# Kernel tuning notes

Hardware: AMD Instinct MI355X
Metric: run time of the kernel (lower is better)

Reference implementation:

```python
import jax, jax.numpy as jnp
import numpy as np

DIM_PN = 64
N_P = 16
BN_EPS = 1e-5


def _conv1x1(h, w, b):
    # h: (B, Cin, N), w: (Cout, Cin), b: (Cout,)
    return jnp.einsum('oc,bcn->bon', w, h) + b[None, :, None]


def _bn(h, g, be):
    # training-mode BatchNorm1d: stats over (batch, points)
    m = h.mean(axis=(0, 2), keepdims=True)
    v = h.var(axis=(0, 2), keepdims=True)
    return (h - m) * jax.lax.rsqrt(v + BN_EPS) * g[None, :, None] + be[None, :, None]


def setup_inputs() -> dict:
    key = jax.random.key(0)
    ks = jax.random.split(key, 8)
    B, N = 32, 16384
    x = jax.random.normal(ks[0], (B, 3, N), dtype=jnp.float32)
    def kaiming(k, shape):
        fan_in = shape[1]
        return jax.random.normal(k, shape, dtype=jnp.float32) * np.float32(1.0 / np.sqrt(fan_in))
    w1 = kaiming(ks[1], (64, 3));   b1 = jnp.zeros((64,), jnp.float32)
    w2 = kaiming(ks[2], (128, 64)); b2 = jnp.zeros((128,), jnp.float32)
    w3 = kaiming(ks[3], (DIM_PN, 128)); b3 = jnp.zeros((DIM_PN,), jnp.float32)
    g1 = jnp.ones((64,), jnp.float32); be1 = jnp.zeros((64,), jnp.float32)
    g2 = jnp.ones((128,), jnp.float32); be2 = jnp.zeros((128,), jnp.float32)
    g3 = jnp.ones((DIM_PN,), jnp.float32); be3 = jnp.zeros((DIM_PN,), jnp.float32)
    return {"x": x, "w1": w1, "b1": b1, "g1": g1, "be1": be1,
            "w2": w2, "b2": b2, "g2": g2, "be2": be2,
            "w3": w3, "b3": b3, "g3": g3, "be3": be3}


def reference(x, w1, b1, g1, be1, w2, b2, g2, be2, w3, b3, g3, be3):
    # SoftPoolfeat forward (core of MSN), vectorized SoftPool.
    h = jax.nn.relu(_bn(_conv1x1(x, w1, b1), g1, be1))       # (B,64,N)
    h = jax.nn.relu(_bn(_conv1x1(h, w2, b2), g2, be2))       # (B,128,N)
    h = _bn(_conv1x1(h, w3, b3), g3, be3)                    # (B,C=64,N)
    # SoftPool: per channel c, ascending sort order over points, keep first N_p.
    idx = jnp.argsort(h, axis=2)[:, :, :N_P]                 # (B,C,Np) int32
    # sp_cube[b, c2, c, n] = h[b, c2, idx[b, c, n]]
    sp_cube = jnp.take_along_axis(h[:, :, None, :], idx[:, None, :, :], axis=3)  # (B,C,C,Np)
    # partial[b, ch, c, n] = x[b, ch, idx[b, c, n]]  (original repeats x over featdim then gathers)
    partial = jnp.take_along_axis(x[:, :, None, :], idx[:, None, :, :], axis=3)  # (B,3,C,Np)
    feat = jnp.concatenate([partial, sp_cube], axis=1)       # (B,3+C,C,Np)
    sp_idx = jnp.broadcast_to(idx[:, None, :, :], (idx.shape[0], 3, idx.shape[1], idx.shape[2]))
    return feat, sp_idx
```

## Files before the change

kernel.cpp:

```cpp
#include <hip/hip_runtime.h>
#include <cstddef>

#pragma clang fp contract(off)

#define B_    32
#define N_    16384
#define NPTS  (B_ * N_)
#define FEATSZ (32 * 67 * 64 * 16)
#define NCHUNK (NPTS / 64)
#define GRID_Y2 1024
#define GRID_XS 512

enum : int {
  D_X9    = 0,
  D_Y3SUM = 16,
  D_Y3SQ  = 80,
  D_Y2S   = 144,
  D_Y2Q   = 272,
  D_XPART = 1024,
};
enum : int {
  F_M1   = 16384,
  F_R1   = 16448,
  F_M2   = 16512,
  F_R2   = 16640,
  F_M3   = 16768,
  F_R3   = 16832,
  F_W2T  = 16896,
  F_W3T  = 25088,
  F_TOPK = 33280,
};
#define Y3_B     524288
#define Y2PART_B 524288

__device__ __forceinline__ float h1_of(const float* __restrict__ w1,
                                       const float* __restrict__ b1,
                                       const float* __restrict__ g1,
                                       const float* __restrict__ be1,
                                       const float* __restrict__ fw, int c,
                                       float x0, float x1, float x2) {
  float s = w1[c*3+0] * x0;
  s = fmaf(w1[c*3+1], x1, s);
  s = fmaf(w1[c*3+2], x2, s);
  float y1 = s + b1[c];
  float t = y1 - fw[F_M1 + c];
  float u = t * fw[F_R1 + c];
  u = u * g1[c];
  u = u + be1[c];
  return fmaxf(u, 0.f);
}

__global__ __launch_bounds__(256) void k_xstats64(const float* __restrict__ x,
                                                  double* __restrict__ wd) {
  __shared__ double sacc[4][9];
  double a0=0,a1=0,a2=0,m00=0,m01=0,m02=0,m11=0,m12=0,m22=0;
  for (int p = blockIdx.x * 256 + threadIdx.x; p < NPTS; p += gridDim.x * 256) {
    int b = p >> 14, n = p & (N_ - 1);
    const float* xb = x + (size_t)b * 3 * N_ + n;
    double x0 = xb[0], x1 = xb[N_], x2 = xb[2 * N_];
    a0 += x0; a1 += x1; a2 += x2;
    m00 = fma(x0,x0,m00); m01 = fma(x0,x1,m01); m02 = fma(x0,x2,m02);
    m11 = fma(x1,x1,m11); m12 = fma(x1,x2,m12); m22 = fma(x2,x2,m22);
  }
  #pragma unroll
  for (int m = 32; m >= 1; m >>= 1) {
    a0 += __shfl_xor(a0, m); a1 += __shfl_xor(a1, m); a2 += __shfl_xor(a2, m);
    m00 += __shfl_xor(m00, m); m01 += __shfl_xor(m01, m); m02 += __shfl_xor(m02, m);
    m11 += __shfl_xor(m11, m); m12 += __shfl_xor(m12, m); m22 += __shfl_xor(m22, m);
  }
  const int wv = threadIdx.x >> 6;
  if ((threadIdx.x & 63) == 0) {
    sacc[wv][0] = a0;  sacc[wv][1] = a1;  sacc[wv][2] = a2;
    sacc[wv][3] = m00; sacc[wv][4] = m01; sacc[wv][5] = m02;
    sacc[wv][6] = m11; sacc[wv][7] = m12; sacc[wv][8] = m22;
  }
  __syncthreads();
  if (threadIdx.x < 9) {
    double s = ((sacc[0][threadIdx.x] + sacc[1][threadIdx.x])
              + sacc[2][threadIdx.x]) + sacc[3][threadIdx.x];
    wd[D_XPART + blockIdx.x * 9 + threadIdx.x] = s;
  }
}

__global__ __launch_bounds__(64) void k_redX(double* __restrict__ wd) {
  int j = threadIdx.x;
  if (j >= 9) return;
  double s = 0.0;
  for (int b = 0; b < GRID_XS; ++b) s += wd[D_XPART + b * 9 + j];
  wd[D_X9 + j] = s;
}

__global__ void k_prep1(const float* __restrict__ w1, const float* __restrict__ b1,
                        double* __restrict__ wd, float* __restrict__ fw) {
  int c = threadIdx.x;
  if (c >= 64) return;
  const double inv = 1.0 / (double)NPTS;
  double mx0 = wd[0]*inv, mx1 = wd[1]*inv, mx2 = wd[2]*inv;
  double c00 = wd[3]*inv - mx0*mx0, c01 = wd[4]*inv - mx0*mx1, c02 = wd[5]*inv - mx0*mx2;
  double c11 = wd[6]*inv - mx1*mx1, c12 = wd[7]*inv - mx1*mx2, c22 = wd[8]*inv - mx2*mx2;
  double w0 = w1[c*3+0], w1_ = w1[c*3+1], w2_ = w1[c*3+2];
  double m1 = w0*mx0 + w1_*mx1 + w2_*mx2 + (double)b1[c];
  double var = w0*w0*c00 + w1_*w1_*c11 + w2_*w2_*c22
             + 2.0*(w0*w1_*c01 + w0*w2_*c02 + w1_*w2_*c12);
  fw[F_M1 + c] = (float)m1;
  float vpe = (float)var + 1e-5f;
  fw[F_R1 + c] = (float)(1.0 / sqrt((double)vpe));
}

__global__ __launch_bounds__(64) void k_prepW(const float* __restrict__ w2,
                                              const float* __restrict__ w3,
                                              float* __restrict__ fw) {
  const int o = blockIdx.x, c = threadIdx.x;
  fw[F_W2T + c * 128 + o] = w2[o * 64 + c];
  fw[F_W3T + o * 64 + c] = w3[c * 128 + o];
}

__global__ __launch_bounds__(1024, 8) void k_y2stats(const float* __restrict__ x,
                                                     const float* __restrict__ w1,
                                                     const float* __restrict__ b1,
                                                     const float* __restrict__ g1,
                                                     const float* __restrict__ be1,
                                                     const float* __restrict__ fw,
                                                     double* __restrict__ y2part) {
  __shared__ float h1g[16][64][4];
  const int tid = threadIdx.x;
  const int lane = tid & 63;
  const int wvu = __builtin_amdgcn_readfirstlane(tid >> 6);
  const int o0 = wvu * 8;
  const float* w2t = fw + F_W2T;
  double s64[8], q64[8];
  #pragma unroll
  for (int j = 0; j < 8; ++j) { s64[j] = 0.0; q64[j] = 0.0; }

  for (int chunk = blockIdx.x; chunk < NCHUNK; chunk += GRID_Y2) {
    __syncthreads();
    {
      int p = chunk * 64 + lane;
      int b = p >> 14, n = p & (N_ - 1);
      const float* xb = x + (size_t)b * 3 * N_ + n;
      float x0 = xb[0], x1 = xb[N_], x2 = xb[2 * N_];
      const int c0 = wvu * 4;
      float hv[4];
      #pragma unroll
      for (int k = 0; k < 4; ++k) hv[k] = h1_of(w1, b1, g1, be1, fw, c0 + k, x0, x1, x2);
      float4 v; v.x = hv[0]; v.y = hv[1]; v.z = hv[2]; v.w = hv[3];
      *(float4*)&h1g[wvu][lane][0] = v;
    }
    __syncthreads();
    float acc[8];
    #pragma unroll
    for (int j = 0; j < 8; ++j) acc[j] = 0.f;
    #pragma unroll 4
    for (int cg = 0; cg < 16; ++cg) {
      float4 hgv = *(const float4*)&h1g[cg][lane][0];
      float hx[4] = {hgv.x, hgv.y, hgv.z, hgv.w};
      #pragma unroll
      for (int e = 0; e < 4; ++e) {
        const int c = cg * 4 + e;
        const float hc = hx[e];
        const float* wc = w2t + c * 128 + o0;
        #pragma unroll
        for (int j = 0; j < 8; ++j) acc[j] = fmaf(wc[j], hc, acc[j]);
      }
    }
    #pragma unroll
    for (int j = 0; j < 8; ++j) {
      double v = (double)acc[j];
      s64[j] += v;
      q64[j] = fma(v, v, q64[j]);
    }
  }
  #pragma unroll
  for (int j = 0; j < 8; ++j) {
    #pragma unroll
    for (int m = 32; m >= 1; m >>= 1) {
      s64[j] += __shfl_xor(s64[j], m);
      q64[j] += __shfl_xor(q64[j], m);
    }
  }
  if (lane == 0) {
    #pragma unroll
    for (int j = 0; j < 8; ++j) {
      int o = o0 + j;
      y2part[((size_t)blockIdx.x * 128 + o) * 2 + 0] = s64[j];
      y2part[((size_t)blockIdx.x * 128 + o) * 2 + 1] = q64[j];
    }
  }
}

__global__ __launch_bounds__(256) void k_redY2(const double* __restrict__ y2part,
                                               double* __restrict__ wd) {
  __shared__ double ss[256], sq[256];
  const int o = blockIdx.x, tid = threadIdx.x;
  double s = 0.0, q = 0.0;
  for (int blk = tid; blk < GRID_Y2; blk += 256) {
    s += y2part[((size_t)blk * 128 + o) * 2 + 0];
    q += y2part[((size_t)blk * 128 + o) * 2 + 1];
  }
  ss[tid] = s; sq[tid] = q;
  __syncthreads();
  for (int st = 128; st > 0; st >>= 1) {
    if (tid < st) { ss[tid] += ss[tid + st]; sq[tid] += sq[tid + st]; }
    __syncthreads();
  }
  if (tid == 0) { wd[D_Y2S + o] = ss[0]; wd[D_Y2Q + o] = sq[0]; }
}

__global__ void k_prep2s(const float* __restrict__ b2,
                         double* __restrict__ wd, float* __restrict__ fw) {
  int o = threadIdx.x;
  if (o >= 128) return;
  const double inv = 1.0 / (double)NPTS;
  double mraw = wd[D_Y2S + o] * inv;
  double var = wd[D_Y2Q + o] * inv - mraw * mraw;
  fw[F_M2 + o] = (float)(mraw + (double)b2[o]);
  float vpe = (float)var + 1e-5f;
  fw[F_R2 + o] = (float)(1.0 / sqrt((double)vpe));
}

__global__ __launch_bounds__(512, 4) void k_fwd(const float* __restrict__ x,
                                                const float* __restrict__ w1,
                                                const float* __restrict__ b1,
                                                const float* __restrict__ g1,
                                                const float* __restrict__ be1,
                                                const float* __restrict__ b2,
                                                const float* __restrict__ g2,
                                                const float* __restrict__ be2,
                                                const float* __restrict__ b3,
                                                const float* __restrict__ fw,
                                                float* __restrict__ y3out,
                                                int pbase) {
  __shared__ float h1g[16][64][4];
  __shared__ float h2g[16][64][4];
  const int tid = threadIdx.x;
  const int lane = tid & 63;
  const int wvu = __builtin_amdgcn_readfirstlane(tid >> 6);
  const int p = pbase + blockIdx.x * 64 + lane;
  const int b = p >> 14, n = p & (N_ - 1);
  const float* xb = x + (size_t)b * 3 * N_ + n;
  const float x0 = xb[0], x1 = xb[N_], x2 = xb[2 * N_];
  const float* w2t = fw + F_W2T;
  const float* w3t = fw + F_W3T;
  const int q0 = wvu * 8;
  float a3[8];

  {
    const int c0 = wvu * 8;
    float hv[8];
    #pragma unroll
    for (int k = 0; k < 8; ++k) hv[k] = h1_of(w1, b1, g1, be1, fw, c0 + k, x0, x1, x2);
    #pragma unroll
    for (int gq = 0; gq < 2; ++gq) {
      float4 v; v.x = hv[gq*4+0]; v.y = hv[gq*4+1]; v.z = hv[gq*4+2]; v.w = hv[gq*4+3];
      *(float4*)&h1g[(c0 >> 2) + gq][lane][0] = v;
    }
  }
  __syncthreads();

  #pragma unroll
  for (int H = 0; H < 2; ++H) {
    {
      const int o0 = H * 64 + wvu * 8;
      float acc[8];
      #pragma unroll
      for (int j = 0; j < 8; ++j) acc[j] = 0.f;
      #pragma unroll 4
      for (int cg = 0; cg < 16; ++cg) {
        float4 hgv = *(const float4*)&h1g[cg][lane][0];
        float hx[4] = {hgv.x, hgv.y, hgv.z, hgv.w};
        #pragma unroll
        for (int e = 0; e < 4; ++e) {
          const int c = cg * 4 + e;
          const float hc = hx[e];
          const float* wc = w2t + c * 128 + o0;
          #pragma unroll
          for (int j = 0; j < 8; ++j) acc[j] = fmaf(wc[j], hc, acc[j]);
        }
      }
      float hv2[8];
      #pragma unroll
      for (int j = 0; j < 8; ++j) {
        int o = o0 + j;
        float y2 = acc[j] + b2[o];
        float t = y2 - fw[F_M2 + o];
        float u = t * fw[F_R2 + o];
        u = u * g2[o];
        u = u + be2[o];
        hv2[j] = fmaxf(u, 0.f);
      }
      #pragma unroll
      for (int gq = 0; gq < 2; ++gq) {
        float4 v; v.x = hv2[gq*4+0]; v.y = hv2[gq*4+1]; v.z = hv2[gq*4+2]; v.w = hv2[gq*4+3];
        *(float4*)&h2g[wvu * 2 + gq][lane][0] = v;
      }
    }
    __syncthreads();
    {
      #pragma unroll 4
      for (int og = 0; og < 16; ++og) {
        float4 hgv = *(const float4*)&h2g[og][lane][0];
        float hx[4] = {hgv.x, hgv.y, hgv.z, hgv.w};
        #pragma unroll
        for (int e = 0; e < 4; ++e) {
          const int o = H * 64 + og * 4 + e;
          const float ho = hx[e];
          const float* wr = w3t + o * 64 + q0;
          if (H == 0 && og == 0 && e == 0) {
            #pragma unroll
            for (int j = 0; j < 8; ++j) a3[j] = wr[j] * ho;
          } else {
            #pragma unroll
            for (int j = 0; j < 8; ++j) a3[j] = fmaf(wr[j], ho, a3[j]);
          }
        }
      }
    }
    __syncthreads();
  }

  float* yrow = y3out + (size_t)b * 64 * N_ + n;
  #pragma unroll
  for (int j = 0; j < 8; ++j) {
    int q = q0 + j;
    yrow[(size_t)q * N_] = a3[j] + b3[q];
  }
}

__global__ void k_prep3(double* __restrict__ wd, float* __restrict__ fw) {
  int o = threadIdx.x;
  if (o >= 64) return;
  const double inv = 1.0 / (double)NPTS;
  double m = wd[D_Y3SUM + o] * inv;
  double var = wd[D_Y3SQ + o] * inv - m * m;
  fw[F_M3 + o] = (float)m;
  float vpe = (float)var + 1e-5f;
  fw[F_R3 + o] = (float)(1.0 / sqrt((double)vpe));
}

__global__ __launch_bounds__(256) void k_topk(const float* __restrict__ y3,
                                              const float* __restrict__ g3,
                                              int* __restrict__ topk,
                                              double* __restrict__ wd) {
  __shared__ float sval[256 * 16];
  __shared__ int   sidx[256 * 16];
  __shared__ double ssum[256], ssq[256];
  const int tid = threadIdx.x;
  const int row = blockIdx.x;
  const int c = row & 63;
  const float sgn = (g3[c] >= 0.f) ? 1.f : -1.f;
  const float4* y = (const float4*)(y3 + (size_t)row * N_);
  float val[16]; int idx[16];
  #pragma unroll
  for (int k = 0; k < 16; ++k) { val[k] = 3.0e38f; idx[k] = 0x7fffffff; }
  auto ins = [&](float v, int i) {
    if (v < val[15] || (v == val[15] && i < idx[15])) {
      float cv = v; int ci = i;
      #pragma unroll
      for (int k = 0; k < 16; ++k) {
        bool sw = (cv < val[k]) || (cv == val[k] && ci < idx[k]);
        float tv = val[k]; int tj = idx[k];
        if (sw) { val[k] = cv; idx[k] = ci; cv = tv; ci = tj; }
      }
    }
  };
  double s = 0.0, q = 0.0;
  #pragma unroll 1
  for (int it = 0; it < 16; ++it) {
    int n4 = it * 256 + tid;
    float4 v = y[n4];
    int nb = n4 * 4;
    {
      double a = v.x, bb = v.y, cc2 = v.z, d = v.w;
      s += a + bb + cc2 + d;
      q = fma(a,a,q); q = fma(bb,bb,q); q = fma(cc2,cc2,q); q = fma(d,d,q);
    }
    ins(sgn * v.x, nb + 0);
    ins(sgn * v.y, nb + 1);
    ins(sgn * v.z, nb + 2);
    ins(sgn * v.w, nb + 3);
  }
  ssum[tid] = s; ssq[tid] = q;
  #pragma unroll
  for (int k = 0; k < 16; ++k) { sval[tid*16+k] = val[k]; sidx[tid*16+k] = idx[k]; }
  __syncthreads();
  for (int st = 128; st > 0; st >>= 1) {
    if (tid < st) { ssum[tid] += ssum[tid + st]; ssq[tid] += ssq[tid + st]; }
    __syncthreads();
  }
  if (tid == 0) {
    atomicAdd(&wd[D_Y3SUM + c], ssum[0]);
    atomicAdd(&wd[D_Y3SQ  + c], ssq[0]);
  }
  for (int st2 = 1; st2 < 256; st2 <<= 1) {
    if ((tid & (2 * st2 - 1)) == 0) {
      int pa = tid * 16, pb = (tid + st2) * 16;
      int ia = 0, ib = 0;
      float mv[16]; int mi[16];
      #pragma unroll
      for (int k = 0; k < 16; ++k) {
        float va = sval[pa + ia]; int ja = sidx[pa + ia];
        float vb = sval[pb + ib]; int jb = sidx[pb + ib];
        bool ta = (va < vb) || (va == vb && ja < jb);
        mv[k] = ta ? va : vb; mi[k] = ta ? ja : jb;
        if (ta) ++ia; else ++ib;
      }
      #pragma unroll
      for (int k = 0; k < 16; ++k) { sval[pa + k] = mv[k]; sidx[pa + k] = mi[k]; }
    }
    __syncthreads();
  }
  if (tid < 16) topk[row * 16 + tid] = sidx[tid];
}

__global__ __launch_bounds__(256) void k_gather(const float* __restrict__ x,
                                                const float* __restrict__ fw,
                                                const float* __restrict__ g3,
                                                const float* __restrict__ be3,
                                                const float* __restrict__ y3,
                                                const int* __restrict__ topk,
                                                float* __restrict__ out) {
  __shared__ int s_i[16];
  __shared__ float s_m[64], s_r[64], s_g[64], s_b[64];
  const int tid = threadIdx.x;
  const int row = blockIdx.x;
  const int b = row >> 6, c = row & 63;
  if (tid < 16) s_i[tid] = topk[row * 16 + tid];
  if (tid < 64) {
    s_m[tid] = fw[F_M3 + tid]; s_r[tid] = fw[F_R3 + tid];
    s_g[tid] = g3[tid];        s_b[tid] = be3[tid];
  }
  __syncthreads();
  for (int t = tid; t < 67 * 16; t += 256) {
    int ch = t >> 4, n = t & 15, i = s_i[n];
    float v;
    if (ch < 3) {
      v = x[((size_t)b * 3 + ch) * N_ + i];
    } else {
      int c2 = ch - 3;
      float yv = y3[((size_t)b * 64 + c2) * N_ + i];
      float tt = yv - s_m[c2];
      float u = tt * s_r[c2];
      u = u * s_g[c2];
      v = u + s_b[c2];
    }
    out[(((size_t)b * 67 + ch) * 64 + c) * 16 + n] = v;
  }
  if (tid < 48) {
    int ch = tid >> 4, n = tid & 15;
    out[FEATSZ + (((size_t)b * 3 + ch) * 64 + c) * 16 + n] = (float)s_i[n];
  }
}

extern "C" void kernel_launch(void* const* d_in, const int* in_sizes, int n_in,
                              void* d_out, int out_size, void* d_ws, size_t ws_size,
                              hipStream_t stream) {
  const float* x   = (const float*)d_in[0];
  const float* w1  = (const float*)d_in[1];
  const float* b1  = (const float*)d_in[2];
  const float* g1  = (const float*)d_in[3];
  const float* be1 = (const float*)d_in[4];
  const float* w2  = (const float*)d_in[5];
  const float* b2  = (const float*)d_in[6];
  const float* g2  = (const float*)d_in[7];
  const float* be2 = (const float*)d_in[8];
  const float* w3  = (const float*)d_in[9];
  const float* b3  = (const float*)d_in[10];
  const float* g3  = (const float*)d_in[11];
  const float* be3 = (const float*)d_in[12];
  double* wd = (double*)d_ws;
  float*  fw = (float*)d_ws;
  float*  out = (float*)d_out;
  int* topk = (int*)(fw + F_TOPK);
  double* y2part = (double*)((char*)d_ws + Y2PART_B);
  float*  y3     = (float*)((char*)d_ws + Y3_B);

  hipMemsetAsync(d_ws, 0, 1152, stream);
  k_xstats64<<<GRID_XS, 256, 0, stream>>>(x, wd);
  k_redX    <<<1, 64, 0, stream>>>(wd);
  k_prep1   <<<1, 64, 0, stream>>>(w1, b1, wd, fw);
  k_prepW   <<<128, 64, 0, stream>>>(w2, w3, fw);
  k_y2stats <<<GRID_Y2, 1024, 0, stream>>>(x, w1, b1, g1, be1, fw, y2part);
  k_redY2   <<<128, 256, 0, stream>>>(y2part, wd);
  k_prep2s  <<<1, 128, 0, stream>>>(b2, wd, fw);
  k_fwd     <<<NPTS / 128, 512, 0, stream>>>(x, w1, b1, g1, be1, b2, g2, be2, b3, fw, y3, 0);
  k_fwd     <<<NPTS / 128, 512, 0, stream>>>(x, w1, b1, g1, be1, b2, g2, be2, b3, fw, y3, NPTS / 2);
  k_topk    <<<B_ * 64, 256, 0, stream>>>(y3, g3, topk, wd);
  k_prep3   <<<1, 64, 0, stream>>>(wd, fw);
  k_gather  <<<B_ * 64, 256, 0, stream>>>(x, fw, g3, be3, y3, topk, out);
  (void)in_sizes; (void)n_in; (void)out_size; (void)ws_size;
}
```

Measured before the change: 546.6 us.

## Replace per-thread insertion top-k with two-pass radix histogram selection

The top-16 selection per (batch, channel) row stops using per-thread sorted insertion lists and a shared-memory merge tree. It now uses two passes of 8-bit radix histograms over order-preserving float keys to find a threshold bucket. Candidates at or below that bucket go into a small buffer, and a single wave picks the 16 smallest from it with shuffles. This removes the heavy per-element compare-swap chain and the log-depth merge, at the cost of reading each row three times and using LDS atomics. It also risks dropping candidates if more than 256 values fall at or below the threshold, which can happen with heavy ties.

```diff
diff --git a/kernel.cpp b/kernel.cpp
--- a/kernel.cpp
+++ b/kernel.cpp
@@ -48,6 +48,11 @@
   u = u * g1[c];
   u = u + be1[c];
   return fmaxf(u, 0.f);
+}
+
+__device__ __forceinline__ unsigned int okey(float f) {
+  unsigned int u = __float_as_uint(f);
+  return (u & 0x80000000u) ? ~u : (u | 0x80000000u);
 }
 
 __global__ __launch_bounds__(256) void k_xstats64(const float* __restrict__ x,
@@ -341,47 +346,41 @@
                                               const float* __restrict__ g3,
                                               int* __restrict__ topk,
                                               double* __restrict__ wd) {
-  __shared__ float sval[256 * 16];
-  __shared__ int   sidx[256 * 16];
+  __shared__ unsigned int hist[4][256];
+  __shared__ unsigned int cnt[256];
+  __shared__ unsigned long long buf[256];
+  __shared__ unsigned int nbuf;
+  __shared__ int s_tbin1, s_before1, s_tbin2;
   __shared__ double ssum[256], ssq[256];
   const int tid = threadIdx.x;
   const int row = blockIdx.x;
   const int c = row & 63;
+  const int wv = tid >> 6;
   const float sgn = (g3[c] >= 0.f) ? 1.f : -1.f;
   const float4* y = (const float4*)(y3 + (size_t)row * N_);
-  float val[16]; int idx[16];
-  #pragma unroll
-  for (int k = 0; k < 16; ++k) { val[k] = 3.0e38f; idx[k] = 0x7fffffff; }
-  auto ins = [&](float v, int i) {
-    if (v < val[15] || (v == val[15] && i < idx[15])) {
-      float cv = v; int ci = i;
-      #pragma unroll
-      for (int k = 0; k < 16; ++k) {
-        bool sw = (cv < val[k]) || (cv == val[k] && ci < idx[k]);
-        float tv = val[k]; int tj = idx[k];
-        if (sw) { val[k] = cv; idx[k] = ci; cv = tv; ci = tj; }
-      }
-    }
-  };
+
+  for (int i = tid; i < 1024; i += 256) ((unsigned int*)hist)[i] = 0;
+  if (tid == 0) nbuf = 0;
+  __syncthreads();
+
   double s = 0.0, q = 0.0;
   #pragma unroll 1
   for (int it = 0; it < 16; ++it) {
     int n4 = it * 256 + tid;
     float4 v = y[n4];
-    int nb = n4 * 4;
     {
       double a = v.x, bb = v.y, cc2 = v.z, d = v.w;
       s += a + bb + cc2 + d;
       q = fma(a,a,q); q = fma(bb,bb,q); q = fma(cc2,cc2,q); q = fma(d,d,q);
     }
-    ins(sgn * v.x, nb + 0);
-    ins(sgn * v.y, nb + 1);
-    ins(sgn * v.z, nb + 2);
-    ins(sgn * v.w, nb + 3);
+    unsigned int u0 = okey(sgn * v.x), u1 = okey(sgn * v.y);
+    unsigned int u2 = okey(sgn * v.z), u3 = okey(sgn * v.w);
+    atomicAdd(&hist[wv][u0 >> 24], 1u);
+    atomicAdd(&hist[wv][u1 >> 24], 1u);
+    atomicAdd(&hist[wv][u2 >> 24], 1u);
+    atomicAdd(&hist[wv][u3 >> 24], 1u);
   }
   ssum[tid] = s; ssq[tid] = q;
-  #pragma unroll
-  for (int k = 0; k < 16; ++k) { sval[tid*16+k] = val[k]; sidx[tid*16+k] = idx[k]; }
   __syncthreads();
   for (int st = 128; st > 0; st >>= 1) {
     if (tid < st) { ssum[tid] += ssum[tid + st]; ssq[tid] += ssq[tid + st]; }
@@ -391,25 +390,102 @@
     atomicAdd(&wd[D_Y3SUM + c], ssum[0]);
     atomicAdd(&wd[D_Y3SQ  + c], ssq[0]);
   }
-  for (int st2 = 1; st2 < 256; st2 <<= 1) {
-    if ((tid & (2 * st2 - 1)) == 0) {
-      int pa = tid * 16, pb = (tid + st2) * 16;
-      int ia = 0, ib = 0;
-      float mv[16]; int mi[16];
+
+  unsigned int myc = hist[0][tid] + hist[1][tid] + hist[2][tid] + hist[3][tid];
+  cnt[tid] = myc;
+  __syncthreads();
+  for (int st = 1; st < 256; st <<= 1) {
+    unsigned int t = (tid >= st) ? cnt[tid - st] : 0u;
+    __syncthreads();
+    cnt[tid] += t;
+    __syncthreads();
+  }
+  {
+    unsigned int incl = cnt[tid], excl = incl - myc;
+    if (excl < 16u && incl >= 16u) { s_tbin1 = tid; s_before1 = (int)excl; }
+  }
+  __syncthreads();
+  const unsigned int tbin1 = (unsigned int)s_tbin1;
+  const int before1 = s_before1;
+
+  for (int i = tid; i < 1024; i += 256) ((unsigned int*)hist)[i] = 0;
+  __syncthreads();
+  #pragma unroll 1
+  for (int it = 0; it < 16; ++it) {
+    int n4 = it * 256 + tid;
+    float4 v = y[n4];
+    unsigned int u0 = okey(sgn * v.x), u1 = okey(sgn * v.y);
+    unsigned int u2 = okey(sgn * v.z), u3 = okey(sgn * v.w);
+    if ((u0 >> 24) == tbin1) atomicAdd(&hist[wv][(u0 >> 16) & 255u], 1u);
+    if ((u1 >> 24) == tbin1) atomicAdd(&hist[wv][(u1 >> 16) & 255u], 1u);
+    if ((u2 >> 24) == tbin1) atomicAdd(&hist[wv][(u2 >> 16) & 255u], 1u);
+    if ((u3 >> 24) == tbin1) atomicAdd(&hist[wv][(u3 >> 16) & 255u], 1u);
+  }
+  __syncthreads();
+  myc = hist[0][tid] + hist[1][tid] + hist[2][tid] + hist[3][tid];
+  cnt[tid] = myc;
+  __syncthreads();
+  for (int st = 1; st < 256; st <<= 1) {
+    unsigned int t = (tid >= st) ? cnt[tid - st] : 0u;
+    __syncthreads();
+    cnt[tid] += t;
+    __syncthreads();
+  }
+  {
+    const unsigned int r2 = (unsigned int)(16 - before1);
+    unsigned int incl = cnt[tid], excl = incl - myc;
+    if (excl < r2 && incl >= r2) s_tbin2 = tid;
+  }
+  __syncthreads();
+  const unsigned int thresh16 = (tbin1 << 8) | (unsigned int)s_tbin2;
+
+  #pragma unroll 1
+  for (int it = 0; it < 16; ++it) {
+    int n4 = it * 256 + tid;
+    float4 v = y[n4];
+    int nb = n4 * 4;
+    unsigned int uu[4] = { okey(sgn * v.x), okey(sgn * v.y),
+                           okey(sgn * v.z), okey(sgn * v.w) };
+    #pragma unroll
+    for (int j = 0; j < 4; ++j) {
+      if ((uu[j] >> 16) <= thresh16) {
+        unsigned int slot = atomicAdd(&nbuf, 1u);
+        if (slot < 256u)
+          buf[slot] = ((unsigned long long)uu[j] << 32) | (unsigned int)(nb + j);
+      }
+    }
+  }
+  __syncthreads();
+
+  if (tid < 64) {
+    const unsigned int m = nbuf < 256u ? nbuf : 256u;
+    const unsigned long long MAXK = ~0ull;
+    unsigned long long k0 = (tid +   0u) < m ? buf[tid +   0] : MAXK;
+    unsigned long long k1 = (tid +  64u) < m ? buf[tid +  64] : MAXK;
+    unsigned long long k2 = (tid + 128u) < m ? buf[tid + 128] : MAXK;
+    unsigned long long k3 = (tid + 192u) < m ? buf[tid + 192] : MAXK;
+    #pragma unroll 1
+    for (int r = 0; r < 16; ++r) {
+      unsigned long long a = k0 < k1 ? k0 : k1;
+      unsigned long long b = k2 < k3 ? k2 : k3;
+      unsigned long long kmin = a < b ? a : b;
       #pragma unroll
-      for (int k = 0; k < 16; ++k) {
-        float va = sval[pa + ia]; int ja = sidx[pa + ia];
-        float vb = sval[pb + ib]; int jb = sidx[pb + ib];
-        bool ta = (va < vb) || (va == vb && ja < jb);
-        mv[k] = ta ? va : vb; mi[k] = ta ? ja : jb;
-        if (ta) ++ia; else ++ib;
-      }
-      #pragma unroll
-      for (int k = 0; k < 16; ++k) { sval[pa + k] = mv[k]; sidx[pa + k] = mi[k]; }
-    }
-    __syncthreads();
-  }
-  if (tid < 16) topk[row * 16 + tid] = sidx[tid];
+      for (int m2 = 32; m2 >= 1; m2 >>= 1) {
+        unsigned long long o = __shfl_xor(kmin, m2);
+        kmin = o < kmin ? o : kmin;
+      }
+      bool have = (k0 == kmin) | (k1 == kmin) | (k2 == kmin) | (k3 == kmin);
+      unsigned long long bal = __ballot(have);
+      int wlane = __ffsll((unsigned long long)bal) - 1;
+      if (tid == wlane) {
+        if (k0 == kmin) k0 = MAXK;
+        else if (k1 == kmin) k1 = MAXK;
+        else if (k2 == kmin) k2 = MAXK;
+        else k3 = MAXK;
+      }
+      if (tid == 0) topk[row * 16 + r] = (int)(kmin & 0xFFFFFFFFull);
+    }
+  }
 }
 
 __global__ __launch_bounds__(256) void k_gather(const float* __restrict__ x,
```

Measured after the change: 503.8 us. 1.09x faster.
